# Optimization experiments

Hardware: AMD Instinct MI355X
Metric: run time of the kernel (lower is better)

Reference implementation:

```python
import jax, jax.numpy as jnp
import numpy as np

HEADS = 8


def setup_inputs() -> dict:
    key = jax.random.key(0)
    k1, k2, k3, k4, k5, k6 = jax.random.split(key, 6)
    B, S, E = 2, 2048, 512
    D = E // HEADS
    return {
        "values": jax.random.normal(k1, (B, S, E), dtype=jnp.float32),
        "keys": jax.random.normal(k2, (B, S, E), dtype=jnp.float32),
        "queries": jax.random.normal(k3, (B, S, E), dtype=jnp.float32),
        "mask": jax.random.randint(k4, (B, 1, 1, S), 0, 2, dtype=jnp.int32),
        "W_v": jax.random.normal(k5, (D, D), dtype=jnp.float32) * (1.0 / np.sqrt(D)),
        "W_o": jax.random.normal(k6, (E, E), dtype=jnp.float32) * (1.0 / np.sqrt(E)),
        "b_o": jnp.zeros((E,), dtype=jnp.float32),
    }


def reference(values, keys, queries, mask, W_v, W_o, b_o):
    B, S, E = queries.shape
    H = HEADS
    D = E // H
    # reshape to (b, s, h, d) and apply the SAME W_v linear to v, k, q
    # (faithful to the original, which calls self.values on all three)
    v = jnp.einsum('bshd,ed->bshe', values.reshape(B, -1, H, D), W_v)
    k = jnp.einsum('bshd,ed->bshe', keys.reshape(B, -1, H, D), W_v)
    q = jnp.einsum('bshd,ed->bshe', queries.reshape(B, -1, H, D), W_v)
    # unscaled attention scores (original has no 1/sqrt(d))
    energy = jnp.einsum('bqhd,bkhd->bhqk', q, k)  # (b, h, q, k)
    energy = jnp.where(mask == 0, -jnp.inf, energy)
    attn = jax.nn.softmax(energy, axis=3)
    out = jnp.einsum('bhqk,bkhd->bqhd', attn, v)  # (b, q, h, d)
    out = out.reshape(B, S, E)
    return out @ W_o.T + b_o
```

## Files before the change

### kernel.cpp

```cpp
#include <hip/hip_runtime.h>


#define B_ 2
#define S_ 2048
#define E_ 512
#define H_ 8
#define D_ 64

typedef unsigned short ushort_t;
typedef __attribute__((ext_vector_type(8))) short short8;
typedef __attribute__((ext_vector_type(8))) _Float16 half8;
typedef __attribute__((ext_vector_type(4))) float f32x4;

__device__ __forceinline__ ushort_t f2bs(float x) {
    union { float f; unsigned int u; } a; a.f = x;
    unsigned int u = a.u;
    u += 0x7fffu + ((u >> 16) & 1u);
    return (ushort_t)(u >> 16);
}
__device__ __forceinline__ float bs2f(ushort_t h) {
    union { unsigned int u; float f; } a; a.u = ((unsigned int)h) << 16;
    return a.f;
}
__device__ __forceinline__ ushort_t f2hs(float x) {
    _Float16 h = (_Float16)x;
    ushort_t u; __builtin_memcpy(&u, &h, 2);
    return u;
}
__device__ __forceinline__ void split16(const float4* g, ushort_t* hi, ushort_t* lo) {
    #pragma unroll
    for (int q = 0; q < 4; ++q) {
        float4 f = g[q];
        float vv[4] = {f.x, f.y, f.z, f.w};
        #pragma unroll
        for (int j = 0; j < 4; ++j) {
            ushort_t h = f2bs(vv[j]);
            hi[q * 4 + j] = h;
            lo[q * 4 + j] = f2bs(vv[j] - bs2f(h));
        }
    }
}

__global__ void __launch_bounds__(256) proj_mfma(
    const float* __restrict__ quer, const float* __restrict__ keys,
    const float* __restrict__ vals, const float* __restrict__ Wv,
    ushort_t* __restrict__ qf, ushort_t* __restrict__ kf,
    ushort_t* __restrict__ vt)
{
    __shared__ ushort_t Ah[64 * 72], Al[64 * 72];
    __shared__ ushort_t Bh[64 * 72], Bl[64 * 72];
    const int tens = blockIdx.y;
    const float* src = tens == 0 ? quer : (tens == 1 ? keys : vals);
    const int bx = blockIdx.x;
    const int st = bx & 31, bh = bx >> 5;
    const int b = bh >> 3, h = bh & 7;
    const int s0 = st * 64;
    const int t = threadIdx.x;

    {
        int e = t >> 2, dg = (t & 3) * 16;
        ushort_t th[16], tl[16];
        split16((const float4*)(Wv + e * 64 + dg), th, tl);
        *(uint4*)&Bh[e * 72 + dg] = *(uint4*)th;  *(uint4*)&Bh[e * 72 + dg + 8] = *(uint4*)(th + 8);
        *(uint4*)&Bl[e * 72 + dg] = *(uint4*)tl;  *(uint4*)&Bl[e * 72 + dg + 8] = *(uint4*)(tl + 8);
    }
    {
        int row = t >> 2, cg = (t & 3) * 16;
        const float* g = src + ((size_t)b * S_ + s0 + row) * 512 + h * 64 + cg;
        ushort_t th[16], tl[16];
        split16((const float4*)g, th, tl);
        *(uint4*)&Ah[row * 72 + cg] = *(uint4*)th;  *(uint4*)&Ah[row * 72 + cg + 8] = *(uint4*)(th + 8);
        *(uint4*)&Al[row * 72 + cg] = *(uint4*)tl;  *(uint4*)&Al[row * 72 + cg + 8] = *(uint4*)(tl + 8);
    }
    __syncthreads();

    const int w = t >> 6, lm = t & 15, quad = (t >> 4) & 3;
    f32x4 acc[4];
    #pragma unroll
    for (int nt = 0; nt < 4; ++nt) acc[nt] = (f32x4){0.f, 0.f, 0.f, 0.f};

    #pragma unroll
    for (int kk = 0; kk < 2; ++kk) {
        short8 ah = *(const short8*)&Ah[(w * 16 + lm) * 72 + kk * 32 + quad * 8];
        short8 al = *(const short8*)&Al[(w * 16 + lm) * 72 + kk * 32 + quad * 8];
        #pragma unroll
        for (int nt = 0; nt < 4; ++nt) {
            short8 bh8 = *(const short8*)&Bh[(nt * 16 + lm) * 72 + kk * 32 + quad * 8];
            short8 bl8 = *(const short8*)&Bl[(nt * 16 + lm) * 72 + kk * 32 + quad * 8];
            acc[nt] = __builtin_amdgcn_mfma_f32_16x16x32_bf16(ah, bh8, acc[nt], 0, 0, 0);
            acc[nt] = __builtin_amdgcn_mfma_f32_16x16x32_bf16(al, bh8, acc[nt], 0, 0, 0);
            acc[nt] = __builtin_amdgcn_mfma_f32_16x16x32_bf16(ah, bl8, acc[nt], 0, 0, 0);
        }
    }

    if (tens < 2) {
        ushort_t* dst = tens == 0 ? qf : kf;
        #pragma unroll
        for (int nt = 0; nt < 4; ++nt) {
            #pragma unroll
            for (int r = 0; r < 4; ++r) {
                size_t addr = ((size_t)bh * S_ + s0 + w * 16 + quad * 4 + r) * 64 + nt * 16 + lm;
                dst[addr] = f2hs(acc[nt][r]);
            }
        }
    } else {
        #pragma unroll
        for (int nt = 0; nt < 4; ++nt) {
            unsigned int p0 = (unsigned int)f2bs(acc[nt][0]) | ((unsigned int)f2bs(acc[nt][1]) << 16);
            unsigned int p1 = (unsigned int)f2bs(acc[nt][2]) | ((unsigned int)f2bs(acc[nt][3]) << 16);
            uint2 pk; pk.x = p0; pk.y = p1;
            size_t addr = ((size_t)bh * 64 + nt * 16 + lm) * S_ + s0 + w * 16 + quad * 4;
            *(uint2*)&vt[addr] = pk;
        }
    }
}

__global__ void __launch_bounds__(512, 4) attn_mfma(
    const ushort_t* __restrict__ qf, const ushort_t* __restrict__ kf,
    const ushort_t* __restrict__ vt, const int* __restrict__ mask,
    ushort_t* __restrict__ ctx)
{
    __shared__ ushort_t Ks[2][64 * 72];
    __shared__ ushort_t Vt[2][64 * 72];
    __shared__ ushort_t Ps[8 * 16 * 72];
    __shared__ float    mb[2][64];

    const int bx = blockIdx.x;
    const int qt = bx & 31;
    const int bh = bx >> 5;
    const int b  = bh >> 3;
    const int t  = threadIdx.x;
    const int w  = t >> 6;
    const int wq = w & 3;
    const int ws = w >> 2;
    const int lm = t & 15, quad = (t >> 4) & 3;
    const int q0 = qt * 64;
    const int wbase = w * 16 * 72;

    const int srow = t >> 3;
    const int scg  = (t & 7) * 8;
    const size_t kgbase = ((size_t)bh * S_ + srow) * 64 + scg;
    const size_t vgbase = ((size_t)bh * 64 + srow) * S_ + scg;

    half8 aq[2];
    {
        size_t qrow = ((size_t)bh * S_ + q0 + wq * 16 + lm) * 64 + quad * 8;
        aq[0] = *(const half8*)&qf[qrow];
        aq[1] = *(const half8*)&qf[qrow + 32];
    }
    short8 ones;
    #pragma unroll
    for (int j = 0; j < 8; ++j) ones[j] = (short)0x3F80;

    f32x4 acc[4];
    #pragma unroll
    for (int nt = 0; nt < 4; ++nt) acc[nt] = (f32x4){0.f, 0.f, 0.f, 0.f};
    f32x4 acc_l = (f32x4){0.f, 0.f, 0.f, 0.f};

    {
        *(uint4*)&Ks[0][srow * 72 + scg] = *(const uint4*)&kf[kgbase];
        *(uint4*)&Ks[1][srow * 72 + scg] = *(const uint4*)&kf[kgbase + 4096];
        *(uint4*)&Vt[0][srow * 72 + scg] = *(const uint4*)&vt[vgbase];
        *(uint4*)&Vt[1][srow * 72 + scg] = *(const uint4*)&vt[vgbase + 64];
        if (t < 128) mb[t >> 6][t & 63] = mask[b * S_ + t] ? -64.f : -1e30f;
    }
    __syncthreads();

    for (int is = 0; is < S_ / 128; ++is) {
        const bool pf = (is + 1) < (S_ / 128);

        uint4 pk0, pk1, pv0, pv1; int mnx = 0;
        if (pf) {
            size_t ko = kgbase + (size_t)(2 * (is + 1)) * 4096;
            pk0 = *(const uint4*)&kf[ko];
            pk1 = *(const uint4*)&kf[ko + 4096];
            size_t vo = vgbase + (size_t)(2 * (is + 1)) * 64;
            pv0 = *(const uint4*)&vt[vo];
            pv1 = *(const uint4*)&vt[vo + 64];
            if (t < 128) mnx = mask[b * S_ + (2 * (is + 1)) * 64 + t];
        }

        const ushort_t* Kc = Ks[ws];
        const ushort_t* Vc = Vt[ws];

        #pragma unroll
        for (int nt = 0; nt < 4; ++nt) {
            f32x4 s = (f32x4){0.f, 0.f, 0.f, 0.f};
            #pragma unroll
            for (int kk = 0; kk < 2; ++kk) {
                half8 ak = *(const half8*)&Kc[(nt * 16 + lm) * 72 + kk * 32 + quad * 8];
                s = __builtin_amdgcn_mfma_f32_16x16x32_f16(ak, aq[kk], s, 0, 0, 0);
            }
            f32x4 mv = *(const f32x4*)&mb[ws][nt * 16 + quad * 4];
            float p0 = __expf(s[0] + mv[0]);
            float p1 = __expf(s[1] + mv[1]);
            float p2 = __expf(s[2] + mv[2]);
            float p3 = __expf(s[3] + mv[3]);
            uint2 pkd;
            pkd.x = (unsigned int)f2bs(p0) | ((unsigned int)f2bs(p1) << 16);
            pkd.y = (unsigned int)f2bs(p2) | ((unsigned int)f2bs(p3) << 16);
            *(uint2*)&Ps[wbase + lm * 72 + nt * 16 + quad * 4] = pkd;
        }
        asm volatile("s_waitcnt lgkmcnt(0)" ::: "memory");
        __builtin_amdgcn_sched_barrier(0);

        #pragma unroll
        for (int kk = 0; kk < 2; ++kk) {
            short8 ap = *(const short8*)&Ps[wbase + lm * 72 + kk * 32 + quad * 8];
            #pragma unroll
            for (int nt = 0; nt < 4; ++nt) {
                short8 bv = *(const short8*)&Vc[(nt * 16 + lm) * 72 + kk * 32 + quad * 8];
                acc[nt] = __builtin_amdgcn_mfma_f32_16x16x32_bf16(ap, bv, acc[nt], 0, 0, 0);
            }
            acc_l = __builtin_amdgcn_mfma_f32_16x16x32_bf16(ap, ones, acc_l, 0, 0, 0);
        }

        __syncthreads();
        if (pf) {
            *(uint4*)&Ks[0][srow * 72 + scg] = pk0;
            *(uint4*)&Ks[1][srow * 72 + scg] = pk1;
            *(uint4*)&Vt[0][srow * 72 + scg] = pv0;
            *(uint4*)&Vt[1][srow * 72 + scg] = pv1;
            if (t < 128) mb[t >> 6][t & 63] = mnx ? -64.f : -1e30f;
            __syncthreads();
        }
    }

    float* cf = (float*)Ps;
    const int lane = t & 63;
    __syncthreads();
    if (ws == 1) {
        const int base = (wq * 64 + lane) * 18;
        #pragma unroll
        for (int nt = 0; nt < 4; ++nt) {
            #pragma unroll
            for (int r = 0; r < 4; r += 2) {
                float2 v2; v2.x = acc[nt][r]; v2.y = acc[nt][r + 1];
                *(float2*)&cf[base + nt * 4 + r] = v2;
            }
        }
    }
    __syncthreads();
    if (ws == 0) {
        const int base = (wq * 64 + lane) * 18;
        #pragma unroll
        for (int nt = 0; nt < 4; ++nt) {
            #pragma unroll
            for (int r = 0; r < 4; ++r) acc[nt][r] += cf[base + nt * 4 + r];
        }
    }
    __syncthreads();
    if (ws == 1) {
        const int base = (wq * 64 + lane) * 5;
        #pragma unroll
        for (int r = 0; r < 4; ++r) cf[base + r] = acc_l[r];
    }
    __syncthreads();

    if (ws == 0) {
        const int base = (wq * 64 + lane) * 5;
        #pragma unroll
        for (int r = 0; r < 4; ++r) acc_l[r] += cf[base + r];
        const int h = bh & 7;
        #pragma unroll
        for (int r = 0; r < 4; ++r) {
            float inv = 1.f / acc_l[r];
            int s = q0 + wq * 16 + quad * 4 + r;
            #pragma unroll
            for (int nt = 0; nt < 4; ++nt) {
                int d = nt * 16 + lm;
                ctx[((size_t)b * S_ + s) * E_ + h * D_ + d] = f2bs(acc[nt][r] * inv);
            }
        }
    }
}

__global__ void __launch_bounds__(256) outproj_mfma(
    const ushort_t* __restrict__ ctx, const float* __restrict__ Wo,
    const float* __restrict__ bo, float* __restrict__ out)
{
    __shared__ ushort_t As[64 * 72];
    __shared__ ushort_t Bs[64 * 72];
    const int m0 = blockIdx.x * 64, n0 = blockIdx.y * 64;
    const int t = threadIdx.x;
    const int w = t >> 6, lm = t & 15, quad = (t >> 4) & 3;

    f32x4 acc[4];
    #pragma unroll
    for (int nt = 0; nt < 4; ++nt) acc[nt] = (f32x4){0.f, 0.f, 0.f, 0.f};

    for (int kc = 0; kc < E_ / 64; ++kc) {
        __syncthreads();
        {
            int row = t >> 2, cg = (t & 3) * 16;
            const ushort_t* g = ctx + (size_t)(m0 + row) * E_ + kc * 64 + cg;
            *(uint4*)&As[row * 72 + cg]     = *(const uint4*)g;
            *(uint4*)&As[row * 72 + cg + 8] = *(const uint4*)(g + 8);
        }
        {
            int n = t >> 2, kg = (t & 3) * 16;
            const float4* g = (const float4*)(Wo + (size_t)(n0 + n) * E_ + kc * 64 + kg);
            ushort_t tmp[16];
            #pragma unroll
            for (int q = 0; q < 4; ++q) {
                float4 f = g[q];
                tmp[q * 4 + 0] = f2bs(f.x); tmp[q * 4 + 1] = f2bs(f.y);
                tmp[q * 4 + 2] = f2bs(f.z); tmp[q * 4 + 3] = f2bs(f.w);
            }
            *(uint4*)&Bs[n * 72 + kg]     = *(uint4*)tmp;
            *(uint4*)&Bs[n * 72 + kg + 8] = *(uint4*)(tmp + 8);
        }
        __syncthreads();

        #pragma unroll
        for (int kk = 0; kk < 2; ++kk) {
            short8 a = *(const short8*)&As[(w * 16 + lm) * 72 + kk * 32 + quad * 8];
            #pragma unroll
            for (int nt = 0; nt < 4; ++nt) {
                short8 bb = *(const short8*)&Bs[(nt * 16 + lm) * 72 + kk * 32 + quad * 8];
                acc[nt] = __builtin_amdgcn_mfma_f32_16x16x32_bf16(a, bb, acc[nt], 0, 0, 0);
            }
        }
    }

    #pragma unroll
    for (int nt = 0; nt < 4; ++nt) {
        float bias = bo[n0 + nt * 16 + lm];
        #pragma unroll
        for (int r = 0; r < 4; ++r) {
            int m = m0 + w * 16 + quad * 4 + r;
            out[(size_t)m * E_ + n0 + nt * 16 + lm] = acc[nt][r] + bias;
        }
    }
}

extern "C" void kernel_launch(void* const* d_in, const int* in_sizes, int n_in,
                              void* d_out, int out_size, void* d_ws, size_t ws_size,
                              hipStream_t stream) {
    const float* vals = (const float*)d_in[0];
    const float* keys = (const float*)d_in[1];
    const float* quer = (const float*)d_in[2];
    const int*   mask = (const int*)d_in[3];
    const float* Wv   = (const float*)d_in[4];
    const float* Wo   = (const float*)d_in[5];
    const float* bo   = (const float*)d_in[6];
    float* out = (float*)d_out;

    const size_t N = (size_t)B_ * H_ * S_ * D_;
    ushort_t* ws  = (ushort_t*)d_ws;
    ushort_t* qf  = ws;
    ushort_t* kf  = ws + N;
    ushort_t* vt  = ws + 2 * N;
    ushort_t* ctx = ws + 3 * N;

    proj_mfma<<<dim3(B_ * H_ * (S_ / 64), 3), 256, 0, stream>>>(
        quer, keys, vals, Wv, qf, kf, vt);
    attn_mfma<<<B_ * H_ * (S_ / 64), 512, 0, stream>>>(qf, kf, vt, mask, ctx);
    outproj_mfma<<<dim3((B_ * S_) / 64, E_ / 64), 256, 0, stream>>>(ctx, Wo, bo, out);
}
```

Before: 132.0 us.

## Pre-convert weights once, pipeline split-K outproj, add MFMA priority hints

A new prep kernel converts W_o to bf16 and W_v to hi/lo bf16 once per call, so the projection and output kernels no longer redo that conversion in every block. The output projection moves to 512 threads with two K-halves per block, register prefetch of the next K chunk, and a shared-memory reduction of the partial sums. setprio hints are placed around the MFMA sections of all kernels, and an explicit lgkmcnt wait plus sched barrier is removed from the attention loop. In exchange it adds one extra kernel launch and more workspace, and leaves ordering of the P stores and reads to the compiler.

```diff
diff --git a/kernel.cpp b/kernel.cpp
--- a/kernel.cpp
+++ b/kernel.cpp
@@ -41,9 +41,32 @@
     }
 }
 
+__global__ void __launch_bounds__(256) prep_convert(
+    const float* __restrict__ Wv, const float* __restrict__ Wo,
+    ushort_t* __restrict__ Wvh, ushort_t* __restrict__ Wvl,
+    ushort_t* __restrict__ Wob)
+{
+    const int t = threadIdx.x, bx = blockIdx.x;
+    if (bx < 128) {
+        int g = (bx * 256 + t) * 8;
+        float4 f0 = *(const float4*)(Wo + g);
+        float4 f1 = *(const float4*)(Wo + g + 4);
+        ushort_t tmp[8] = {f2bs(f0.x), f2bs(f0.y), f2bs(f0.z), f2bs(f0.w),
+                           f2bs(f1.x), f2bs(f1.y), f2bs(f1.z), f2bs(f1.w)};
+        *(uint4*)&Wob[g] = *(uint4*)tmp;
+    } else {
+        int g = t * 16;
+        ushort_t th[16], tl[16];
+        split16((const float4*)(Wv + g), th, tl);
+        *(uint4*)&Wvh[g]     = *(uint4*)th;  *(uint4*)&Wvh[g + 8] = *(uint4*)(th + 8);
+        *(uint4*)&Wvl[g]     = *(uint4*)tl;  *(uint4*)&Wvl[g + 8] = *(uint4*)(tl + 8);
+    }
+}
+
 __global__ void __launch_bounds__(256) proj_mfma(
     const float* __restrict__ quer, const float* __restrict__ keys,
-    const float* __restrict__ vals, const float* __restrict__ Wv,
+    const float* __restrict__ vals,
+    const ushort_t* __restrict__ Wvh, const ushort_t* __restrict__ Wvl,
     ushort_t* __restrict__ qf, ushort_t* __restrict__ kf,
     ushort_t* __restrict__ vt)
 {
@@ -59,10 +82,10 @@
 
     {
         int e = t >> 2, dg = (t & 3) * 16;
-        ushort_t th[16], tl[16];
-        split16((const float4*)(Wv + e * 64 + dg), th, tl);
-        *(uint4*)&Bh[e * 72 + dg] = *(uint4*)th;  *(uint4*)&Bh[e * 72 + dg + 8] = *(uint4*)(th + 8);
-        *(uint4*)&Bl[e * 72 + dg] = *(uint4*)tl;  *(uint4*)&Bl[e * 72 + dg + 8] = *(uint4*)(tl + 8);
+        *(uint4*)&Bh[e * 72 + dg]     = *(const uint4*)&Wvh[e * 64 + dg];
+        *(uint4*)&Bh[e * 72 + dg + 8] = *(const uint4*)&Wvh[e * 64 + dg + 8];
+        *(uint4*)&Bl[e * 72 + dg]     = *(const uint4*)&Wvl[e * 64 + dg];
+        *(uint4*)&Bl[e * 72 + dg + 8] = *(const uint4*)&Wvl[e * 64 + dg + 8];
     }
     {
         int row = t >> 2, cg = (t & 3) * 16;
@@ -79,6 +102,7 @@
     #pragma unroll
     for (int nt = 0; nt < 4; ++nt) acc[nt] = (f32x4){0.f, 0.f, 0.f, 0.f};
 
+    __builtin_amdgcn_s_setprio(1);
     #pragma unroll
     for (int kk = 0; kk < 2; ++kk) {
         short8 ah = *(const short8*)&Ah[(w * 16 + lm) * 72 + kk * 32 + quad * 8];
@@ -92,6 +116,7 @@
             acc[nt] = __builtin_amdgcn_mfma_f32_16x16x32_bf16(ah, bl8, acc[nt], 0, 0, 0);
         }
     }
+    __builtin_amdgcn_s_setprio(0);
 
     if (tens < 2) {
         ushort_t* dst = tens == 0 ? qf : kf;
@@ -186,11 +211,13 @@
         #pragma unroll
         for (int nt = 0; nt < 4; ++nt) {
             f32x4 s = (f32x4){0.f, 0.f, 0.f, 0.f};
+            __builtin_amdgcn_s_setprio(1);
             #pragma unroll
             for (int kk = 0; kk < 2; ++kk) {
                 half8 ak = *(const half8*)&Kc[(nt * 16 + lm) * 72 + kk * 32 + quad * 8];
                 s = __builtin_amdgcn_mfma_f32_16x16x32_f16(ak, aq[kk], s, 0, 0, 0);
             }
+            __builtin_amdgcn_s_setprio(0);
             f32x4 mv = *(const f32x4*)&mb[ws][nt * 16 + quad * 4];
             float p0 = __expf(s[0] + mv[0]);
             float p1 = __expf(s[1] + mv[1]);
@@ -201,9 +228,8 @@
             pkd.y = (unsigned int)f2bs(p2) | ((unsigned int)f2bs(p3) << 16);
             *(uint2*)&Ps[wbase + lm * 72 + nt * 16 + quad * 4] = pkd;
         }
-        asm volatile("s_waitcnt lgkmcnt(0)" ::: "memory");
-        __builtin_amdgcn_sched_barrier(0);
-
+
+        __builtin_amdgcn_s_setprio(1);
         #pragma unroll
         for (int kk = 0; kk < 2; ++kk) {
             short8 ap = *(const short8*)&Ps[wbase + lm * 72 + kk * 32 + quad * 8];
@@ -214,6 +240,7 @@
             }
             acc_l = __builtin_amdgcn_mfma_f32_16x16x32_bf16(ap, ones, acc_l, 0, 0, 0);
         }
+        __builtin_amdgcn_s_setprio(0);
 
         __syncthreads();
         if (pf) {
@@ -275,61 +302,90 @@
     }
 }
 
-__global__ void __launch_bounds__(256) outproj_mfma(
-    const ushort_t* __restrict__ ctx, const float* __restrict__ Wo,
+__global__ void __launch_bounds__(512, 4) outproj_mfma(
+    const ushort_t* __restrict__ ctx, const ushort_t* __restrict__ Wob,
     const float* __restrict__ bo, float* __restrict__ out)
 {
-    __shared__ ushort_t As[64 * 72];
-    __shared__ ushort_t Bs[64 * 72];
+    __shared__ ushort_t sm[4][64 * 72];
     const int m0 = blockIdx.x * 64, n0 = blockIdx.y * 64;
     const int t = threadIdx.x;
-    const int w = t >> 6, lm = t & 15, quad = (t >> 4) & 3;
+    const int w = t >> 6, wq = w & 3, wk = w >> 2;
+    const int lm = t & 15, quad = (t >> 4) & 3;
+    const int srow = t >> 3, scg = (t & 7) * 8;
+
+    const size_t abase = (size_t)(m0 + srow) * E_ + scg;
+    const size_t bbase = (size_t)(n0 + srow) * E_ + scg;
 
     f32x4 acc[4];
     #pragma unroll
     for (int nt = 0; nt < 4; ++nt) acc[nt] = (f32x4){0.f, 0.f, 0.f, 0.f};
 
-    for (int kc = 0; kc < E_ / 64; ++kc) {
+    *(uint4*)&sm[0][srow * 72 + scg] = *(const uint4*)&ctx[abase];
+    *(uint4*)&sm[1][srow * 72 + scg] = *(const uint4*)&ctx[abase + 256];
+    *(uint4*)&sm[2][srow * 72 + scg] = *(const uint4*)&Wob[bbase];
+    *(uint4*)&sm[3][srow * 72 + scg] = *(const uint4*)&Wob[bbase + 256];
+    __syncthreads();
+
+    const ushort_t* Ac = sm[wk];
+    const ushort_t* Bc = sm[2 + wk];
+
+    for (int is = 0; is < 4; ++is) {
+        const bool pf = is < 3;
+        uint4 pa0, pa1, pb0, pb1;
+        if (pf) {
+            pa0 = *(const uint4*)&ctx[abase + (size_t)(is + 1) * 64];
+            pa1 = *(const uint4*)&ctx[abase + 256 + (size_t)(is + 1) * 64];
+            pb0 = *(const uint4*)&Wob[bbase + (size_t)(is + 1) * 64];
+            pb1 = *(const uint4*)&Wob[bbase + 256 + (size_t)(is + 1) * 64];
+        }
+
+        __builtin_amdgcn_s_setprio(1);
+        #pragma unroll
+        for (int kk = 0; kk < 2; ++kk) {
+            short8 a = *(const short8*)&Ac[(wq * 16 + lm) * 72 + kk * 32 + quad * 8];
+            #pragma unroll
+            for (int nt = 0; nt < 4; ++nt) {
+                short8 bb = *(const short8*)&Bc[(nt * 16 + lm) * 72 + kk * 32 + quad * 8];
+                acc[nt] = __builtin_amdgcn_mfma_f32_16x16x32_bf16(a, bb, acc[nt], 0, 0, 0);
+            }
+        }
+        __builtin_amdgcn_s_setprio(0);
+
         __syncthreads();
-        {
-            int row = t >> 2, cg = (t & 3) * 16;
-            const ushort_t* g = ctx + (size_t)(m0 + row) * E_ + kc * 64 + cg;
-            *(uint4*)&As[row * 72 + cg]     = *(const uint4*)g;
-            *(uint4*)&As[row * 72 + cg + 8] = *(const uint4*)(g + 8);
-        }
-        {
-            int n = t >> 2, kg = (t & 3) * 16;
-            const float4* g = (const float4*)(Wo + (size_t)(n0 + n) * E_ + kc * 64 + kg);
-            ushort_t tmp[16];
-            #pragma unroll
-            for (int q = 0; q < 4; ++q) {
-                float4 f = g[q];
-                tmp[q * 4 + 0] = f2bs(f.x); tmp[q * 4 + 1] = f2bs(f.y);
-                tmp[q * 4 + 2] = f2bs(f.z); tmp[q * 4 + 3] = f2bs(f.w);
-            }
-            *(uint4*)&Bs[n * 72 + kg]     = *(uint4*)tmp;
-            *(uint4*)&Bs[n * 72 + kg + 8] = *(uint4*)(tmp + 8);
-        }
-        __syncthreads();
-
-        #pragma unroll
-        for (int kk = 0; kk < 2; ++kk) {
-            short8 a = *(const short8*)&As[(w * 16 + lm) * 72 + kk * 32 + quad * 8];
-            #pragma unroll
-            for (int nt = 0; nt < 4; ++nt) {
-                short8 bb = *(const short8*)&Bs[(nt * 16 + lm) * 72 + kk * 32 + quad * 8];
-                acc[nt] = __builtin_amdgcn_mfma_f32_16x16x32_bf16(a, bb, acc[nt], 0, 0, 0);
-            }
-        }
-    }
-
-    #pragma unroll
-    for (int nt = 0; nt < 4; ++nt) {
-        float bias = bo[n0 + nt * 16 + lm];
-        #pragma unroll
-        for (int r = 0; r < 4; ++r) {
-            int m = m0 + w * 16 + quad * 4 + r;
-            out[(size_t)m * E_ + n0 + nt * 16 + lm] = acc[nt][r] + bias;
+        if (pf) {
+            *(uint4*)&sm[0][srow * 72 + scg] = pa0;
+            *(uint4*)&sm[1][srow * 72 + scg] = pa1;
+            *(uint4*)&sm[2][srow * 72 + scg] = pb0;
+            *(uint4*)&sm[3][srow * 72 + scg] = pb1;
+            __syncthreads();
+        }
+    }
+
+    float* cf = (float*)sm;
+    const int lane = t & 63;
+    if (wk == 1) {
+        const int base = (wq * 64 + lane) * 18;
+        #pragma unroll
+        for (int nt = 0; nt < 4; ++nt) {
+            #pragma unroll
+            for (int r = 0; r < 4; r += 2) {
+                float2 v2; v2.x = acc[nt][r]; v2.y = acc[nt][r + 1];
+                *(float2*)&cf[base + nt * 4 + r] = v2;
+            }
+        }
+    }
+    __syncthreads();
+    if (wk == 0) {
+        const int base = (wq * 64 + lane) * 18;
+        #pragma unroll
+        for (int nt = 0; nt < 4; ++nt) {
+            float bias = bo[n0 + nt * 16 + lm];
+            #pragma unroll
+            for (int r = 0; r < 4; ++r) {
+                int m = m0 + wq * 16 + quad * 4 + r;
+                out[(size_t)m * E_ + n0 + nt * 16 + lm] =
+                    acc[nt][r] + cf[base + nt * 4 + r] + bias;
+            }
         }
     }
 }
@@ -352,9 +408,13 @@
     ushort_t* kf  = ws + N;
     ushort_t* vt  = ws + 2 * N;
     ushort_t* ctx = ws + 3 * N;
-
+    ushort_t* Wob = ws + 4 * N;
+    ushort_t* Wvh = Wob + 512 * 512;
+    ushort_t* Wvl = Wvh + 64 * 64;
+
+    prep_convert<<<129, 256, 0, stream>>>(Wv, Wo, Wvh, Wvl, Wob);
     proj_mfma<<<dim3(B_ * H_ * (S_ / 64), 3), 256, 0, stream>>>(
-        quer, keys, vals, Wv, qf, kf, vt);
+        quer, keys, vals, Wvh, Wvl, qf, kf, vt);
     attn_mfma<<<B_ * H_ * (S_ / 64), 512, 0, stream>>>(qf, kf, vt, mask, ctx);
-    outproj_mfma<<<dim3((B_ * S_) / 64, E_ / 64), 256, 0, stream>>>(ctx, Wo, bo, out);
-}
+    outproj_mfma<<<dim3((B_ * S_) / 64, E_ / 64), 512, 0, stream>>>(ctx, Wob, bo, out);
+}
```

Result: no change. 129.7 us (-1.8%).
